# Kernel optimization log

Measured on AMD Instinct MI355X. Metric: run time of the kernel, lower is better.

## Reference

```python
import jax, jax.numpy as jnp
import numpy as np

B, H, W, C = 16, 32, 32, 256
N = H * W


def setup_inputs() -> dict:
    key = jax.random.key(0)
    ks = jax.random.split(key, 8)
    x = jax.random.normal(ks[0], (B, H, W, C), dtype=jnp.float32)
    # nn.LazyLinear(C): weight (C, C), bias (C,)
    scale = 1.0 / np.sqrt(C)
    Wq = jax.random.uniform(ks[1], (C, C), jnp.float32, -scale, scale)
    bq = jax.random.uniform(ks[2], (C,), jnp.float32, -scale, scale)
    Wk = jax.random.uniform(ks[3], (C, C), jnp.float32, -scale, scale)
    bk = jax.random.uniform(ks[4], (C,), jnp.float32, -scale, scale)
    Wv = jax.random.uniform(ks[5], (C, C), jnp.float32, -scale, scale)
    bv = jax.random.uniform(ks[6], (C,), jnp.float32, -scale, scale)
    # torch.randn(H, H*W, W)
    Wp = jax.random.normal(ks[7], (H, N, W), dtype=jnp.float32)
    return {"x": x, "Wq": Wq, "bq": bq, "Wk": Wk, "bk": bk,
            "Wv": Wv, "bv": bv, "Wp": Wp}


def reference(x, Wq, bq, Wk, bk, Wv, bv, Wp):
    b, h, w, c = x.shape
    n = h * w
    # Linear projections (torch Linear: x @ W^T + b), flatten spatial dims to N tokens
    q = (jnp.einsum('bhwc,dc->bhwd', x, Wq) + bq).reshape(b, n, c)
    k = (jnp.einsum('bhwc,dc->bhwd', x, Wk) + bk).reshape(b, n, c)
    v = (jnp.einsum('bhwc,dc->bhwd', x, Wv) + bv).reshape(b, n, c)
    # Unscaled attention over the N spatial tokens (no 1/sqrt(C) in the original)
    scores = jnp.einsum('bnc,bmc->bnm', q, k)          # (B, N, N)
    attn = jax.nn.softmax(scores, axis=-1)
    qkv = jnp.einsum('bnm,bmc->bnc', attn, v)           # (B, N, C)
    # z = (qkv^T [B,1,C,N] @ Wp [H,N,W]).transpose(-2,-1) -> (B, H, W, C)
    z = jnp.einsum('bnc,hnw->bhwc', qkv, Wp)
    return z
```

## Files before the change

kernel.cpp:

```cpp
#include <hip/hip_runtime.h>
#include <hip/hip_bf16.h>

#define BB 16
#define NN 1024
#define CC 256

typedef __attribute__((ext_vector_type(8))) short bf16x8;
typedef __attribute__((ext_vector_type(4))) short s16x4;
typedef __attribute__((ext_vector_type(4))) float f32x4;

#define GPTR(p) ((const __attribute__((address_space(1))) void*)(p))
#define LPTR(p) ((__attribute__((address_space(3))) void*)(p))

__device__ __forceinline__ unsigned short f2bf(float f) {
  union { float f; unsigned u; } v; v.f = f;
  unsigned r = v.u + 0x7FFFu + ((v.u >> 16) & 1u);
  return (unsigned short)(r >> 16);
}

#define NCAST 17155
__global__ __launch_bounds__(256) void preprocess(
    const float* __restrict__ x,
    const float* __restrict__ Wq, const float* __restrict__ Wk,
    const float* __restrict__ Wv,
    const float* __restrict__ bq, const float* __restrict__ bk,
    const float* __restrict__ bv,
    const float* __restrict__ Wp,
    unsigned short* __restrict__ xb,
    unsigned short* __restrict__ wqkvb,
    float* __restrict__ bqkv,
    unsigned short* __restrict__ Amat) {
  __shared__ float tile[32][33];
  int blk = blockIdx.x;
  if (blk < NCAST) {
    const int NX = BB * NN * CC;
    const int NW = CC * CC;
    int i = blk * 256 + threadIdx.x;
    if (i < NX) { xb[i] = f2bf(x[i]); return; }
    int j = i - NX;
    if (j < 3 * NW) {
      const float* w = (j < NW) ? Wq : (j < 2 * NW ? Wk : Wv);
      wqkvb[j] = f2bf(w[j % NW]);
      return;
    }
    int jj = j - 3 * NW;
    if (jj < 3 * CC) {
      const float* bb = (jj < CC) ? bq : (jj < 2 * CC ? bk : bv);
      bqkv[jj] = bb[jj % CC];
    }
    return;
  }
  int wb = blk - NCAST;
  int h = wb >> 5;
  int n0 = (wb & 31) * 32;
#pragma unroll
  for (int j = 0; j < 4; j++) {
    int idx = threadIdx.x + j * 256;
    int a = idx >> 5, wc = idx & 31;
    tile[a][wc] = Wp[(size_t)h * (NN * 32) + (size_t)(n0 + a) * 32 + wc];
  }
  __syncthreads();
#pragma unroll
  for (int j = 0; j < 4; j++) {
    int idx = threadIdx.x + j * 256;
    int wc = idx >> 5, a = idx & 31;
    Amat[(size_t)(h * 32 + wc) * NN + n0 + a] = f2bf(tile[a][wc]);
  }
}

template <int BIAS_MODE, int F32OUT>
__global__ __launch_bounds__(256) void gemm_tile(
    const unsigned short* __restrict__ A, int lda, long sA,
    const unsigned short* __restrict__ Bt, int ldb, long sB,
    const float* __restrict__ bias,
    void* __restrict__ Out, int ldo, long sO, int K) {
  __shared__ unsigned short As[2 * 128 * 32];
  __shared__ unsigned short Bs[2 * 64 * 32];
  int b = blockIdx.x;
  int m0 = blockIdx.y * 128;
  int n0 = blockIdx.z * 64;
  int t = threadIdx.x;
  int w = t >> 6, lane = t & 63;
  int wm = (w >> 1) * 64, wn = (w & 1) * 32;
  int r = lane & 15, g = lane >> 4;

  const unsigned short* Ab = A + (long)b * sA;
  const unsigned short* Bb = Bt + (long)b * sB;

  int srow = t >> 2;
  int scol = (t & 3) * 8;

  f32x4 acc[4][2];
#pragma unroll
  for (int i = 0; i < 4; i++)
#pragma unroll
    for (int j = 0; j < 2; j++) acc[i][j] = (f32x4){0.f, 0.f, 0.f, 0.f};

  for (int k0 = 0; k0 < K; k0 += 64) {
    __syncthreads();
#pragma unroll
    for (int kh = 0; kh < 2; kh++) {
#pragma unroll
      for (int jj = 0; jj < 2; jj++) {
        __builtin_amdgcn_global_load_lds(
            GPTR(Ab + (long)(m0 + srow + jj * 64) * lda + k0 + kh * 32 + scol),
            LPTR(&As[kh * 4096 + jj * 2048 + t * 8]), 16, 0, 0);
      }
      __builtin_amdgcn_global_load_lds(
          GPTR(Bb + (long)(n0 + srow) * ldb + k0 + kh * 32 + scol),
          LPTR(&Bs[kh * 2048 + t * 8]), 16, 0, 0);
    }
    __syncthreads();
#pragma unroll
    for (int kh = 0; kh < 2; kh++) {
      bf16x8 af[4], bfr[2];
#pragma unroll
      for (int ti = 0; ti < 4; ti++)
        af[ti] = *(const bf16x8*)&As[kh * 4096 + (wm + ti * 16 + r) * 32 + g * 8];
#pragma unroll
      for (int tj = 0; tj < 2; tj++)
        bfr[tj] = *(const bf16x8*)&Bs[kh * 2048 + (wn + tj * 16 + r) * 32 + g * 8];
#pragma unroll
      for (int ti = 0; ti < 4; ti++)
#pragma unroll
        for (int tj = 0; tj < 2; tj++)
          acc[ti][tj] = __builtin_amdgcn_mfma_f32_16x16x32_bf16(af[ti], bfr[tj], acc[ti][tj], 0, 0, 0);
    }
  }

#pragma unroll
  for (int ti = 0; ti < 4; ti++) {
#pragma unroll
    for (int tj = 0; tj < 2; tj++) {
      int col = n0 + wn + tj * 16 + r;
      float bc = (BIAS_MODE == 1) ? bias[col] : 0.0f;
#pragma unroll
      for (int rr = 0; rr < 4; rr++) {
        int row = m0 + wm + ti * 16 + g * 4 + rr;
        float val = acc[ti][tj][rr] + bc;
        long oidx = (long)b * sO + (long)row * ldo + col;
        if (F32OUT)
          ((float*)Out)[oidx] = val;
        else
          ((unsigned short*)Out)[oidx] = f2bf(val);
      }
    }
  }
}

__global__ __launch_bounds__(256) void gemm_qkv(
    const unsigned short* __restrict__ A,
    const unsigned short* __restrict__ Bt,
    const float* __restrict__ bias,
    unsigned short* __restrict__ Qb, unsigned short* __restrict__ Kb,
    unsigned short* __restrict__ Vtb) {
  __shared__ unsigned short As[2 * 128 * 32];
  __shared__ unsigned short Bs[2 * 128 * 32];
  int b = blockIdx.x;
  int m0 = blockIdx.y * 128;
  int n0 = blockIdx.z * 128;
  int t = threadIdx.x;
  int w = t >> 6, lane = t & 63;
  int wm = (w >> 1) * 64, wn = (w & 1) * 64;
  int r = lane & 15, g = lane >> 4;

  const unsigned short* Ab = A + (long)b * NN * CC;
  int srow = t >> 2;
  int scol = (t & 3) * 8;

  f32x4 acc[4][4];
#pragma unroll
  for (int i = 0; i < 4; i++)
#pragma unroll
    for (int j = 0; j < 4; j++) acc[i][j] = (f32x4){0.f, 0.f, 0.f, 0.f};

  for (int k0 = 0; k0 < CC; k0 += 64) {
    __syncthreads();
#pragma unroll
    for (int kh = 0; kh < 2; kh++) {
#pragma unroll
      for (int jj = 0; jj < 2; jj++) {
        __builtin_amdgcn_global_load_lds(
            GPTR(Ab + (long)(m0 + srow + jj * 64) * CC + k0 + kh * 32 + scol),
            LPTR(&As[kh * 4096 + jj * 2048 + t * 8]), 16, 0, 0);
        __builtin_amdgcn_global_load_lds(
            GPTR(Bt + (long)(n0 + srow + jj * 64) * CC + k0 + kh * 32 + scol),
            LPTR(&Bs[kh * 4096 + jj * 2048 + t * 8]), 16, 0, 0);
      }
    }
    __syncthreads();
#pragma unroll
    for (int kh = 0; kh < 2; kh++) {
      bf16x8 af[4], bfr[4];
#pragma unroll
      for (int ti = 0; ti < 4; ti++)
        af[ti] = *(const bf16x8*)&As[kh * 4096 + (wm + ti * 16 + r) * 32 + g * 8];
#pragma unroll
      for (int tj = 0; tj < 4; tj++)
        bfr[tj] = *(const bf16x8*)&Bs[kh * 4096 + (wn + tj * 16 + r) * 32 + g * 8];
#pragma unroll
      for (int ti = 0; ti < 4; ti++)
#pragma unroll
        for (int tj = 0; tj < 4; tj++)
          acc[ti][tj] = __builtin_amdgcn_mfma_f32_16x16x32_bf16(af[ti], bfr[tj], acc[ti][tj], 0, 0, 0);
    }
  }

  int seg = n0 >> 8;
#pragma unroll
  for (int ti = 0; ti < 4; ti++) {
#pragma unroll
    for (int tj = 0; tj < 4; tj++) {
      int col = n0 + wn + tj * 16 + r;
      int c = col & 255;
      float bc = bias[col];
#pragma unroll
      for (int rr = 0; rr < 4; rr++) {
        int row = m0 + wm + ti * 16 + g * 4 + rr;
        float val = acc[ti][tj][rr] + bc;
        long base = (long)b * NN * CC;
        if (seg == 0) {
          Qb[base + (long)row * CC + c] = f2bf(val);
        } else if (seg == 1) {
          Kb[base + ((long)(c >> 5) * NN + row) * 32 + (c & 31)] = f2bf(val);
        } else {
          Vtb[base + ((((long)(c >> 4) * 128 + (row >> 3)) * 16 + (c & 15)) * 8 + (row & 7))] = f2bf(val);
        }
      }
    }
  }
}

__global__ __launch_bounds__(512, 2) void attn_fused(
    const unsigned short* __restrict__ Q,
    const unsigned short* __restrict__ Kt,
    const unsigned short* __restrict__ Vt,
    unsigned short* __restrict__ QKVt) {
  __shared__ unsigned short ShBuf[64 * 1024];
  __shared__ float red[8][64];
  int b = blockIdx.x;
  int n0 = blockIdx.y * 64;
  int t = threadIdx.x;
  int w = t >> 6, lane = t & 63;
  int r = lane & 15, g = lane >> 4;

  const unsigned short* kslab = Kt + (long)b * NN * CC + w * 128 * 32;
  unsigned short* wbuf0 = &ShBuf[w * 4096];
  unsigned short* wbuf1 = &ShBuf[32768 + w * 4096];

  const unsigned short* qbase = Q + ((long)b * NN + n0 + r) * CC + g * 8;

#pragma unroll
  for (int j = 0; j < 8; j++)
    __builtin_amdgcn_global_load_lds(GPTR(kslab + j * 512 + lane * 8),
                                     LPTR(wbuf0 + j * 512 + lane * 8), 16, 0, 0);
  bf16x8 qa[4];
#pragma unroll
  for (int rt = 0; rt < 4; rt++)
    qa[rt] = *(const bf16x8*)(qbase + rt * 16 * CC);

  f32x4 acc[4][8];
#pragma unroll
  for (int i = 0; i < 4; i++)
#pragma unroll
    for (int j = 0; j < 8; j++) acc[i][j] = (f32x4){0.f, 0.f, 0.f, 0.f};

#pragma unroll
  for (int kk = 0; kk < 8; kk++) {
    unsigned short* cur = (kk & 1) ? wbuf1 : wbuf0;
    unsigned short* nxt = (kk & 1) ? wbuf0 : wbuf1;
    if (kk < 7) {
      const unsigned short* src = kslab + (long)(kk + 1) * (NN * 32);
#pragma unroll
      for (int j = 0; j < 8; j++)
        __builtin_amdgcn_global_load_lds(GPTR(src + j * 512 + lane * 8),
                                         LPTR(nxt + j * 512 + lane * 8), 16, 0, 0);
      asm volatile("s_waitcnt vmcnt(8)" ::: "memory");
    } else {
      asm volatile("s_waitcnt vmcnt(0)" ::: "memory");
    }
    __builtin_amdgcn_sched_barrier(0);
    bf16x8 qn[4];
    if (kk < 7) {
#pragma unroll
      for (int rt = 0; rt < 4; rt++)
        qn[rt] = *(const bf16x8*)(qbase + (kk + 1) * 32 + rt * 16 * CC);
    }
#pragma unroll
    for (int ct = 0; ct < 8; ct++) {
      bf16x8 kf = *(const bf16x8*)&cur[(ct * 16 + r) * 32 + g * 8];
#pragma unroll
      for (int rt = 0; rt < 4; rt++)
        acc[rt][ct] = __builtin_amdgcn_mfma_f32_16x16x32_bf16(qa[rt], kf, acc[rt][ct], 0, 0, 0);
    }
    if (kk < 7) {
#pragma unroll
      for (int rt = 0; rt < 4; rt++) qa[rt] = qn[rt];
    }
    __builtin_amdgcn_sched_barrier(0);
  }

  float mrow[4][4];
#pragma unroll
  for (int rt = 0; rt < 4; rt++) {
#pragma unroll
    for (int rr = 0; rr < 4; rr++) {
      float m = acc[rt][0][rr];
#pragma unroll
      for (int ct = 1; ct < 8; ct++) m = fmaxf(m, acc[rt][ct][rr]);
#pragma unroll
      for (int d = 1; d < 16; d <<= 1) m = fmaxf(m, __shfl_xor(m, d, 64));
      mrow[rt][rr] = m;
    }
  }
  if (r == 0) {
#pragma unroll
    for (int rt = 0; rt < 4; rt++)
#pragma unroll
      for (int rr = 0; rr < 4; rr++)
        red[w][rt * 16 + g * 4 + rr] = mrow[rt][rr];
  }
  __syncthreads();
#pragma unroll
  for (int rt = 0; rt < 4; rt++) {
#pragma unroll
    for (int rr = 0; rr < 4; rr++) {
      int row = rt * 16 + g * 4 + rr;
      float m = red[0][row];
#pragma unroll
      for (int w2 = 1; w2 < 8; w2++) m = fmaxf(m, red[w2][row]);
      mrow[rt][rr] = m;
    }
  }
  __syncthreads();
  float ssum[4][4];
#pragma unroll
  for (int rt = 0; rt < 4; rt++) {
#pragma unroll
    for (int rr = 0; rr < 4; rr++) {
      float s = 0.f;
#pragma unroll
      for (int ct = 0; ct < 8; ct++) {
        float e = exp2f((acc[rt][ct][rr] - mrow[rt][rr]) * 1.44269504088896f);
        acc[rt][ct][rr] = e;
        s += e;
      }
#pragma unroll
      for (int d = 1; d < 16; d <<= 1) s += __shfl_xor(s, d, 64);
      ssum[rt][rr] = s;
    }
  }
  if (r == 0) {
#pragma unroll
    for (int rt = 0; rt < 4; rt++)
#pragma unroll
      for (int rr = 0; rr < 4; rr++)
        red[w][rt * 16 + g * 4 + rr] = ssum[rt][rr];
  }
  __syncthreads();
#pragma unroll
  for (int rt = 0; rt < 4; rt++) {
#pragma unroll
    for (int rr = 0; rr < 4; rr++) {
      int prow = rt * 16 + g * 4 + rr;
      float s = 0.f;
#pragma unroll
      for (int w2 = 0; w2 < 8; w2++) s += red[w2][prow];
      float inv = 1.0f / s;
      int sw = prow & 7;
#pragma unroll
      for (int ct = 0; ct < 8; ct++) {
        int col = w * 128 + ct * 16 + r;
        int chunk = (col >> 3) ^ sw;
        ShBuf[prow * 1024 + chunk * 8 + (col & 7)] = f2bf(acc[rt][ct][rr] * inv);
      }
    }
  }
  __syncthreads();

  const unsigned short* vbase = Vt + (long)b * NN * CC;
  int cw = w * 32;
  f32x4 o[4][2];
#pragma unroll
  for (int i = 0; i < 4; i++)
#pragma unroll
    for (int j = 0; j < 2; j++) o[i][j] = (f32x4){0.f, 0.f, 0.f, 0.f};

#pragma unroll 4
  for (int m0 = 0; m0 < NN; m0 += 32) {
    bf16x8 ar[4], br[2];
#pragma unroll
    for (int bt = 0; bt < 2; bt++) {
      long vidx = (((long)((cw >> 4) + bt) * 128 + (m0 >> 3) + g) * 16 + r) * 8;
      br[bt] = *(const bf16x8*)(vbase + vidx);
    }
#pragma unroll
    for (int rt = 0; rt < 4; rt++) {
      int prow = rt * 16 + r;
      int chunk = ((m0 >> 3) + g) ^ (prow & 7);
      ar[rt] = *(const bf16x8*)&ShBuf[prow * 1024 + chunk * 8];
    }
#pragma unroll
    for (int rt = 0; rt < 4; rt++)
#pragma unroll
      for (int bt = 0; bt < 2; bt++)
        o[rt][bt] = __builtin_amdgcn_mfma_f32_16x16x32_bf16(ar[rt], br[bt], o[rt][bt], 0, 0, 0);
  }

  unsigned short* obase = QKVt + (long)b * NN * CC;
#pragma unroll
  for (int rt = 0; rt < 4; rt++) {
#pragma unroll
    for (int bt = 0; bt < 2; bt++) {
      int c = cw + bt * 16 + r;
      int n = n0 + rt * 16 + g * 4;
      s16x4 pk;
      pk.x = (short)f2bf(o[rt][bt][0]);
      pk.y = (short)f2bf(o[rt][bt][1]);
      pk.z = (short)f2bf(o[rt][bt][2]);
      pk.w = (short)f2bf(o[rt][bt][3]);
      *(s16x4*)(obase + (long)c * NN + n) = pk;
    }
  }
}

extern "C" void kernel_launch(void* const* d_in, const int* in_sizes, int n_in,
                              void* d_out, int out_size, void* d_ws, size_t ws_size,
                              hipStream_t stream) {
  const float* x  = (const float*)d_in[0];
  const float* Wq = (const float*)d_in[1];
  const float* bq = (const float*)d_in[2];
  const float* Wk = (const float*)d_in[3];
  const float* bk = (const float*)d_in[4];
  const float* Wv = (const float*)d_in[5];
  const float* bv = (const float*)d_in[6];
  const float* Wp = (const float*)d_in[7];
  float* out = (float*)d_out;

  const long BNC = (long)BB * NN * CC;

  char* p = (char*)d_ws;
  unsigned short* xb    = (unsigned short*)p; p += BNC * 2;
  unsigned short* wqkvb = (unsigned short*)p; p += 3L * CC * CC * 2;
  float*          bqkv  = (float*)p;          p += 4096;
  unsigned short* Amat  = (unsigned short*)p; p += (long)NN * NN * 2;
  unsigned short* Qb    = (unsigned short*)p; p += BNC * 2;
  unsigned short* Ktb   = (unsigned short*)p; p += BNC * 2;
  unsigned short* Vtb   = (unsigned short*)p; p += BNC * 2;
  unsigned short* QKVt  = (unsigned short*)p; p += BNC * 2;

  preprocess<<<NCAST + 1024, 256, 0, stream>>>(
      x, Wq, Wk, Wv, bq, bk, bv, Wp, xb, wqkvb, bqkv, Amat);

  gemm_qkv<<<dim3(BB, 8, 6), 256, 0, stream>>>(xb, wqkvb, bqkv, Qb, Ktb, Vtb);

  attn_fused<<<dim3(BB, NN / 64), 512, 0, stream>>>(Qb, Ktb, Vtb, QKVt);

  gemm_tile<0, 1><<<dim3(BB, 8, 4), 256, 0, stream>>>(
      Amat, NN, 0L, QKVt, NN, (long)NN * CC, nullptr,
      out, CC, (long)NN * CC, NN);
}
```

Before: 156.0 us.

## Fuse fp32-to-bf16 casting and Wp transpose into the QKV GEMM kernel

Removes the separate preprocess kernel. The QKV GEMM now reads fp32 x and weights directly, converts them to bf16 in registers and stores them to LDS, prefetching the next x tile in registers. The Wp transpose moves into extra blocks (z==6) of the same launch. The attention kernel also gains s_setprio around its MFMA loops and a one-step register prefetch of V fragments. This saves a launch and a full bf16 round trip of x through memory. In exchange the GEMM does more global fp32 traffic per tile, loses the async global_load_lds path, and runs uneven transpose blocks alongside the GEMM blocks.

```diff
diff --git a/kernel.cpp b/kernel.cpp
--- a/kernel.cpp
+++ b/kernel.cpp
@@ -18,54 +18,13 @@
   return (unsigned short)(r >> 16);
 }
 
-#define NCAST 17155
-__global__ __launch_bounds__(256) void preprocess(
-    const float* __restrict__ x,
-    const float* __restrict__ Wq, const float* __restrict__ Wk,
-    const float* __restrict__ Wv,
-    const float* __restrict__ bq, const float* __restrict__ bk,
-    const float* __restrict__ bv,
-    const float* __restrict__ Wp,
-    unsigned short* __restrict__ xb,
-    unsigned short* __restrict__ wqkvb,
-    float* __restrict__ bqkv,
-    unsigned short* __restrict__ Amat) {
-  __shared__ float tile[32][33];
-  int blk = blockIdx.x;
-  if (blk < NCAST) {
-    const int NX = BB * NN * CC;
-    const int NW = CC * CC;
-    int i = blk * 256 + threadIdx.x;
-    if (i < NX) { xb[i] = f2bf(x[i]); return; }
-    int j = i - NX;
-    if (j < 3 * NW) {
-      const float* w = (j < NW) ? Wq : (j < 2 * NW ? Wk : Wv);
-      wqkvb[j] = f2bf(w[j % NW]);
-      return;
-    }
-    int jj = j - 3 * NW;
-    if (jj < 3 * CC) {
-      const float* bb = (jj < CC) ? bq : (jj < 2 * CC ? bk : bv);
-      bqkv[jj] = bb[jj % CC];
-    }
-    return;
-  }
-  int wb = blk - NCAST;
-  int h = wb >> 5;
-  int n0 = (wb & 31) * 32;
-#pragma unroll
-  for (int j = 0; j < 4; j++) {
-    int idx = threadIdx.x + j * 256;
-    int a = idx >> 5, wc = idx & 31;
-    tile[a][wc] = Wp[(size_t)h * (NN * 32) + (size_t)(n0 + a) * 32 + wc];
-  }
-  __syncthreads();
-#pragma unroll
-  for (int j = 0; j < 4; j++) {
-    int idx = threadIdx.x + j * 256;
-    int wc = idx >> 5, a = idx & 31;
-    Amat[(size_t)(h * 32 + wc) * NN + n0 + a] = f2bf(tile[a][wc]);
-  }
+__device__ __forceinline__ bf16x8 pack8(f32x4 a, f32x4 b) {
+  bf16x8 o;
+  o[0] = (short)f2bf(a[0]); o[1] = (short)f2bf(a[1]);
+  o[2] = (short)f2bf(a[2]); o[3] = (short)f2bf(a[3]);
+  o[4] = (short)f2bf(b[0]); o[5] = (short)f2bf(b[1]);
+  o[6] = (short)f2bf(b[2]); o[7] = (short)f2bf(b[3]);
+  return o;
 }
 
 template <int BIAS_MODE, int F32OUT>
@@ -149,13 +108,43 @@
 }
 
 __global__ __launch_bounds__(256) void gemm_qkv(
-    const unsigned short* __restrict__ A,
-    const unsigned short* __restrict__ Bt,
-    const float* __restrict__ bias,
+    const float* __restrict__ x,
+    const float* __restrict__ Wq, const float* __restrict__ Wk,
+    const float* __restrict__ Wv,
+    const float* __restrict__ bq, const float* __restrict__ bk,
+    const float* __restrict__ bv,
+    const float* __restrict__ Wp,
     unsigned short* __restrict__ Qb, unsigned short* __restrict__ Kb,
-    unsigned short* __restrict__ Vtb) {
+    unsigned short* __restrict__ Vtb, unsigned short* __restrict__ Amat) {
   __shared__ unsigned short As[2 * 128 * 32];
   __shared__ unsigned short Bs[2 * 128 * 32];
+  __shared__ float tile[32][33];
+
+  if (blockIdx.z == 6) {
+    int id = blockIdx.x * 8 + blockIdx.y;
+#pragma unroll 1
+    for (int u = 0; u < 8; u++) {
+      int wb = id * 8 + u;
+      int h = wb >> 5;
+      int n0w = (wb & 31) * 32;
+#pragma unroll
+      for (int j = 0; j < 4; j++) {
+        int idx = threadIdx.x + j * 256;
+        int a = idx >> 5, wc = idx & 31;
+        tile[a][wc] = Wp[(size_t)h * (NN * 32) + (size_t)(n0w + a) * 32 + wc];
+      }
+      __syncthreads();
+#pragma unroll
+      for (int j = 0; j < 4; j++) {
+        int idx = threadIdx.x + j * 256;
+        int wc = idx >> 5, a = idx & 31;
+        Amat[(size_t)(h * 32 + wc) * NN + n0w + a] = f2bf(tile[a][wc]);
+      }
+      __syncthreads();
+    }
+    return;
+  }
+
   int b = blockIdx.x;
   int m0 = blockIdx.y * 128;
   int n0 = blockIdx.z * 128;
@@ -164,15 +153,35 @@
   int wm = (w >> 1) * 64, wn = (w & 1) * 64;
   int r = lane & 15, g = lane >> 4;
 
-  const unsigned short* Ab = A + (long)b * NN * CC;
+  const float* Ab = x + (long)b * NN * CC;
   int srow = t >> 2;
   int scol = (t & 3) * 8;
 
+  const float* Wsel[2];
+  int wrow[2];
+#pragma unroll
+  for (int jj = 0; jj < 2; jj++) {
+    int nbase = n0 + jj * 64;
+    int seg = nbase >> 8;
+    Wsel[jj] = (seg == 0) ? Wq : (seg == 1 ? Wk : Wv);
+    wrow[jj] = (nbase + srow) & 255;
+  }
+
   f32x4 acc[4][4];
 #pragma unroll
   for (int i = 0; i < 4; i++)
 #pragma unroll
     for (int j = 0; j < 4; j++) acc[i][j] = (f32x4){0.f, 0.f, 0.f, 0.f};
+
+  f32x4 pa[4][2];
+#pragma unroll
+  for (int kh = 0; kh < 2; kh++)
+#pragma unroll
+    for (int jj = 0; jj < 2; jj++) {
+      const float* src = Ab + (long)(m0 + srow + jj * 64) * CC + kh * 32 + scol;
+      pa[kh * 2 + jj][0] = *(const f32x4*)src;
+      pa[kh * 2 + jj][1] = *(const f32x4*)(src + 4);
+    }
 
   for (int k0 = 0; k0 < CC; k0 += 64) {
     __syncthreads();
@@ -180,15 +189,26 @@
     for (int kh = 0; kh < 2; kh++) {
 #pragma unroll
       for (int jj = 0; jj < 2; jj++) {
-        __builtin_amdgcn_global_load_lds(
-            GPTR(Ab + (long)(m0 + srow + jj * 64) * CC + k0 + kh * 32 + scol),
-            LPTR(&As[kh * 4096 + jj * 2048 + t * 8]), 16, 0, 0);
-        __builtin_amdgcn_global_load_lds(
-            GPTR(Bt + (long)(n0 + srow + jj * 64) * CC + k0 + kh * 32 + scol),
-            LPTR(&Bs[kh * 4096 + jj * 2048 + t * 8]), 16, 0, 0);
+        const float* wsrc = Wsel[jj] + (long)wrow[jj] * CC + k0 + kh * 32 + scol;
+        f32x4 b0 = *(const f32x4*)wsrc;
+        f32x4 b1 = *(const f32x4*)(wsrc + 4);
+        *(bf16x8*)&Bs[kh * 4096 + jj * 2048 + t * 8] = pack8(b0, b1);
+        *(bf16x8*)&As[kh * 4096 + jj * 2048 + t * 8] =
+            pack8(pa[kh * 2 + jj][0], pa[kh * 2 + jj][1]);
       }
     }
     __syncthreads();
+    if (k0 < CC - 64) {
+#pragma unroll
+      for (int kh = 0; kh < 2; kh++)
+#pragma unroll
+        for (int jj = 0; jj < 2; jj++) {
+          const float* src =
+              Ab + (long)(m0 + srow + jj * 64) * CC + k0 + 64 + kh * 32 + scol;
+          pa[kh * 2 + jj][0] = *(const f32x4*)src;
+          pa[kh * 2 + jj][1] = *(const f32x4*)(src + 4);
+        }
+    }
 #pragma unroll
     for (int kh = 0; kh < 2; kh++) {
       bf16x8 af[4], bfr[4];
@@ -206,6 +226,8 @@
     }
   }
 
+  int sege = (n0 + wn) >> 8;
+  const float* bsel = (sege == 0) ? bq : (sege == 1 ? bk : bv);
   int seg = n0 >> 8;
 #pragma unroll
   for (int ti = 0; ti < 4; ti++) {
@@ -213,7 +235,7 @@
     for (int tj = 0; tj < 4; tj++) {
       int col = n0 + wn + tj * 16 + r;
       int c = col & 255;
-      float bc = bias[col];
+      float bc = bsel[c];
 #pragma unroll
       for (int rr = 0; rr < 4; rr++) {
         int row = m0 + wm + ti * 16 + g * 4 + rr;
@@ -286,6 +308,7 @@
       for (int rt = 0; rt < 4; rt++)
         qn[rt] = *(const bf16x8*)(qbase + (kk + 1) * 32 + rt * 16 * CC);
     }
+    __builtin_amdgcn_s_setprio(1);
 #pragma unroll
     for (int ct = 0; ct < 8; ct++) {
       bf16x8 kf = *(const bf16x8*)&cur[(ct * 16 + r) * 32 + g * 8];
@@ -293,12 +316,23 @@
       for (int rt = 0; rt < 4; rt++)
         acc[rt][ct] = __builtin_amdgcn_mfma_f32_16x16x32_bf16(qa[rt], kf, acc[rt][ct], 0, 0, 0);
     }
+    __builtin_amdgcn_s_setprio(0);
     if (kk < 7) {
 #pragma unroll
       for (int rt = 0; rt < 4; rt++) qa[rt] = qn[rt];
     }
     __builtin_amdgcn_sched_barrier(0);
   }
+
+  const unsigned short* vbase = Vt + (long)b * NN * CC;
+  int cw = w * 32;
+  bf16x8 brp[2];
+#pragma unroll
+  for (int bt = 0; bt < 2; bt++) {
+    long vidx = (((long)((cw >> 4) + bt) * 128 + g) * 16 + r) * 8;
+    brp[bt] = *(const bf16x8*)(vbase + vidx);
+  }
+  __builtin_amdgcn_sched_barrier(0);
 
   float mrow[4][4];
 #pragma unroll
@@ -378,8 +412,6 @@
   }
   __syncthreads();
 
-  const unsigned short* vbase = Vt + (long)b * NN * CC;
-  int cw = w * 32;
   f32x4 o[4][2];
 #pragma unroll
   for (int i = 0; i < 4; i++)
@@ -389,10 +421,13 @@
 #pragma unroll 4
   for (int m0 = 0; m0 < NN; m0 += 32) {
     bf16x8 ar[4], br[2];
-#pragma unroll
-    for (int bt = 0; bt < 2; bt++) {
-      long vidx = (((long)((cw >> 4) + bt) * 128 + (m0 >> 3) + g) * 16 + r) * 8;
-      br[bt] = *(const bf16x8*)(vbase + vidx);
+    br[0] = brp[0]; br[1] = brp[1];
+    if (m0 + 32 < NN) {
+#pragma unroll
+      for (int bt = 0; bt < 2; bt++) {
+        long vidx = (((long)((cw >> 4) + bt) * 128 + ((m0 + 32) >> 3) + g) * 16 + r) * 8;
+        brp[bt] = *(const bf16x8*)(vbase + vidx);
+      }
     }
 #pragma unroll
     for (int rt = 0; rt < 4; rt++) {
@@ -400,11 +435,13 @@
       int chunk = ((m0 >> 3) + g) ^ (prow & 7);
       ar[rt] = *(const bf16x8*)&ShBuf[prow * 1024 + chunk * 8];
     }
+    __builtin_amdgcn_s_setprio(1);
 #pragma unroll
     for (int rt = 0; rt < 4; rt++)
 #pragma unroll
       for (int bt = 0; bt < 2; bt++)
         o[rt][bt] = __builtin_amdgcn_mfma_f32_16x16x32_bf16(ar[rt], br[bt], o[rt][bt], 0, 0, 0);
+    __builtin_amdgcn_s_setprio(0);
   }
 
   unsigned short* obase = QKVt + (long)b * NN * CC;
@@ -440,19 +477,14 @@
   const long BNC = (long)BB * NN * CC;
 
   char* p = (char*)d_ws;
-  unsigned short* xb    = (unsigned short*)p; p += BNC * 2;
-  unsigned short* wqkvb = (unsigned short*)p; p += 3L * CC * CC * 2;
-  float*          bqkv  = (float*)p;          p += 4096;
   unsigned short* Amat  = (unsigned short*)p; p += (long)NN * NN * 2;
   unsigned short* Qb    = (unsigned short*)p; p += BNC * 2;
   unsigned short* Ktb   = (unsigned short*)p; p += BNC * 2;
   unsigned short* Vtb   = (unsigned short*)p; p += BNC * 2;
   unsigned short* QKVt  = (unsigned short*)p; p += BNC * 2;
 
-  preprocess<<<NCAST + 1024, 256, 0, stream>>>(
-      x, Wq, Wk, Wv, bq, bk, bv, Wp, xb, wqkvb, bqkv, Amat);
-
-  gemm_qkv<<<dim3(BB, 8, 6), 256, 0, stream>>>(xb, wqkvb, bqkv, Qb, Ktb, Vtb);
+  gemm_qkv<<<dim3(BB, 8, 7), 256, 0, stream>>>(
+      x, Wq, Wk, Wv, bq, bk, bv, Wp, Qb, Ktb, Vtb, Amat);
 
   attn_fused<<<dim3(BB, NN / 64), 512, 0, stream>>>(Qb, Ktb, Vtb, QKVt);
 
```

After: 151.5 us. 2.9% less time.
